# Optimization experiments

Measured on AMD Instinct MI355X. Metric: run time of the kernel, lower is better.

Reference implementation:

```python
import jax, jax.numpy as jnp
import numpy as np

HIDDEN, LATENT, SYM, BOX = 512, 256, 64, 128
LEAF = 16384
NODE = 2 * LEAF - 1  # 32767: complete binary tree, leaves first
W_SCALE = 0.05  # keep tanh unsaturated


def setup_inputs() -> dict:
    key = jax.random.key(0)
    ks = jax.random.split(key, 16)
    # kids: valid tree structure (randint per-spec would give invalid child pointers).
    # Leaves are nodes [0, LEAF); internal node LEAF+j merges nodes 2j and 2j+1
    # (1-indexed pointers 2j+1, 2j+2). Every 4th internal node is a symmetry node.
    j = np.arange(NODE - LEAF)
    kids = np.zeros((1, NODE, 3), dtype=np.int32)
    kids[0, LEAF:, 0] = 2 * j + 1
    kids[0, LEAF:, 1] = 2 * j + 2
    kids[0, LEAF:, 2] = (j % 4 == 3).astype(np.int32)
    f32 = jnp.float32
    return {
        "kids": jnp.asarray(kids),
        "shape": jax.random.normal(ks[0], (1, BOX, LEAF), dtype=f32),
        "param": jax.random.normal(ks[1], (1, NODE, SYM), dtype=f32),
        # leaf / box encoder: box -> latent
        "Wb": jax.random.normal(ks[2], (BOX, LATENT), dtype=f32) * W_SCALE,
        "bb": jnp.zeros((LATENT,), dtype=f32),
        # adjacency encoder: (latent, latent) -> hidden -> latent
        "Wl": jax.random.normal(ks[3], (LATENT, HIDDEN), dtype=f32) * W_SCALE,
        "Wr": jax.random.normal(ks[4], (LATENT, HIDDEN), dtype=f32) * W_SCALE,
        "b1": jnp.zeros((HIDDEN,), dtype=f32),
        "W2": jax.random.normal(ks[5], (HIDDEN, LATENT), dtype=f32) * W_SCALE,
        "b2": jnp.zeros((LATENT,), dtype=f32),
        # symmetry encoder: (latent, sym) -> hidden -> latent
        "Wsl": jax.random.normal(ks[6], (LATENT, HIDDEN), dtype=f32) * W_SCALE,
        "Wsr": jax.random.normal(ks[7], (SYM, HIDDEN), dtype=f32) * W_SCALE,
        "bs1": jnp.zeros((HIDDEN,), dtype=f32),
        "Ws2": jax.random.normal(ks[8], (HIDDEN, LATENT), dtype=f32) * W_SCALE,
        "bs2": jnp.zeros((LATENT,), dtype=f32),
    }


def reference(kids, shape, param, Wb, bb, Wl, Wr, b1, W2, b2, Wsl, Wsr, bs1, Ws2, bs2):
    nodeNum = kids.shape[1]
    leafNum = shape.shape[2]
    latent = Wb.shape[1]

    # Leaves (nodes 0..leafNum-1, kids[...,0]==0) have no data dependence on hOut:
    # encode them all at once. boxes: [leafNum, box]
    boxes = jnp.transpose(shape[0])
    hLeaf = jnp.tanh(boxes @ Wb + bb)  # [leafNum, latent]
    hOut = jnp.zeros((nodeNum, latent), dtype=shape.dtype).at[:leafNum].set(hLeaf)

    p = param[0]  # [nodeNum, sym]
    k = kids[0]   # [nodeNum, 3]

    def step(h, x):
        i, k0, k1, k2 = x
        a = h[k0 - 1]      # [latent] left child hidden
        b = h[k1 - 1]      # [latent] right child hidden (adjacency case)
        s = p[k0 - 1]      # [sym]    (source indexes param with kids[...,0]-1)
        # adjacency merge
        h1 = jnp.tanh(jnp.tanh(a @ Wl + b @ Wr + b1) @ W2 + b2)
        # symmetry merge
        h2 = jnp.tanh(jnp.tanh(a @ Wsl + s @ Wsr + bs1) @ Ws2 + bs2)
        hi = jnp.where(k2 == 1, h2, h1)
        return h.at[i].set(hi), None

    # internal nodes are i in [leafNum, nodeNum); original only defines inputs there
    idx = jnp.arange(leafNum, nodeNum)
    xs = (idx, k[leafNum:, 0], k[leafNum:, 1], k[leafNum:, 2])
    hOut, _ = jax.lax.scan(step, hOut, xs)
    return hOut[nodeNum - 1][None, :]  # [1, latent], the root code
```

## Files before the change

### kernel.cpp

```cpp
#include <hip/hip_runtime.h>

#define LEAF   16384
#define NNODE  (2*LEAF-1)
#define LATENT 256
#define HIDDEN 512
#define SYM    64
#define BOX    128

using half8 = __attribute__((ext_vector_type(8))) _Float16;
using f32x4 = __attribute__((ext_vector_type(4))) float;

__device__ __forceinline__ f32x4 mfma16h(half8 a, half8 b, f32x4 c){
    return __builtin_amdgcn_mfma_f32_16x16x32_f16(a, b, c, 0, 0, 0);
}

__global__ void pack_all(const float* __restrict__ Wl, const float* __restrict__ Wr,
                         const float* __restrict__ Wsl, const float* __restrict__ Wsr,
                         const float* __restrict__ W2, const float* __restrict__ Ws2,
                         const float* __restrict__ Wb,
                         _Float16* __restrict__ wcat, _Float16* __restrict__ wscat,
                         _Float16* __restrict__ w2p, _Float16* __restrict__ ws2p,
                         _Float16* __restrict__ wbp)
{
    int g = blockIdx.x*256 + threadIdx.x;
    const float *A, *B; _Float16* pk; int Ksplit, N, KS, t;
    if (g < 262144)      { t = g;          A=Wl;  B=Wr;  pk=wcat;  Ksplit=256; N=512; KS=16; }
    else if (g < 425984) { t = g-262144;   A=Wsl; B=Wsr; pk=wscat; Ksplit=256; N=512; KS=10; }
    else if (g < 557056) { t = g-425984;   A=W2;  B=W2;  pk=w2p;   Ksplit=512; N=256; KS=16; }
    else if (g < 688128) { t = g-557056;   A=Ws2; B=Ws2; pk=ws2p;  Ksplit=512; N=256; KS=16; }
    else if (g < 720896) { t = g-688128;   A=Wb;  B=Wb;  pk=wbp;   Ksplit=128; N=256; KS=4;  }
    else return;
    int j = t & 7, l = (t>>3)&63, tile = (t>>9)&3;
    int rest = t >> 11;
    int ks = rest % KS, cb = rest / KS;
    int k   = ks*32 + ((l>>4)*8) + j;
    int col = cb*64 + tile*16 + (l&15);
    float wv = (k < Ksplit) ? A[(size_t)k*N + col] : B[(size_t)(k-Ksplit)*N + col];
    pk[((size_t)(cb*KS + ks)*4 + tile)*512 + (size_t)l*8 + j] = (_Float16)wv;
}

__global__ __launch_bounds__(256) void leaf_mfma_kernel(
    const float* __restrict__ shape, const _Float16* __restrict__ wbpk,
    const float* __restrict__ bb, _Float16* __restrict__ hh)
{
    const int t = threadIdx.x, lane = t & 63, w = t >> 6;
    const int r0 = blockIdx.x * 64;
    const int m = r0 + w*16 + (lane & 15);

    half8 A[4];
    #pragma unroll
    for (int ks = 0; ks < 4; ++ks) {
        #pragma unroll
        for (int e = 0; e < 8; ++e) {
            int k = ks*32 + (lane >> 4)*8 + e;
            A[ks][e] = (_Float16)shape[(size_t)k*LEAF + m];
        }
    }

    for (int cb = 0; cb < 4; ++cb) {
        f32x4 acc[4];
        #pragma unroll
        for (int c = 0; c < 4; ++c) acc[c] = (f32x4){0.f,0.f,0.f,0.f};
        #pragma unroll
        for (int ks = 0; ks < 4; ++ks) {
            const _Float16* pb = wbpk + (size_t)((cb*4 + ks)*4)*512;
            #pragma unroll
            for (int tile = 0; tile < 4; ++tile) {
                half8 B = *(const half8*)(pb + tile*512 + lane*8);
                acc[tile] = mfma16h(A[ks], B, acc[tile]);
            }
        }
        #pragma unroll
        for (int tile = 0; tile < 4; ++tile) {
            int col = cb*64 + tile*16 + (lane & 15);
            float bv = bb[col];
            #pragma unroll
            for (int r = 0; r < 4; ++r) {
                int row = r0 + w*16 + (lane >> 4)*4 + r;
                hh[(size_t)row*256 + col] = (_Float16)tanhf(acc[tile][r] + bv);
            }
        }
    }
}

template<int NSUB>
__device__ __forceinline__ void k1_body(
    int rb, int cb, int start, int n,
    const _Float16* __restrict__ hh, const float* __restrict__ param,
    const _Float16* __restrict__ wcatpk, const _Float16* __restrict__ wscatpk,
    const float* __restrict__ b1, const float* __restrict__ bs1,
    _Float16* __restrict__ U, _Float16* __restrict__ V)
{
    __shared__ __align__(16) _Float16 ldsB1[2*2048];
    const int t = threadIdx.x, lane = t & 63, w = t >> 6;
    const bool isV = cb >= 8;
    const int cbl = isV ? cb - 8 : cb;
    const int KS  = isV ? 10 : 16;
    const _Float16* pk = (isV ? wscatpk : wcatpk) + (size_t)cbl * KS * 2048;
    const int row0  = rb * NSUB * 64;
    const int cbase = 2 * (start - LEAF);

    f32x4 acc[NSUB][4];
    #pragma unroll
    for (int s = 0; s < NSUB; ++s)
        #pragma unroll
        for (int c = 0; c < 4; ++c) acc[s][c] = (f32x4){0.f,0.f,0.f,0.f};

    *(half8*)(ldsB1 + t*8) = *(const half8*)(pk + (size_t)t*8);
    __syncthreads();

    for (int ks = 0; ks < KS; ++ks) {
        const bool hasNext = ks + 1 < KS;
        half8 stg;
        if (hasNext) stg = *(const half8*)(pk + (size_t)(ks+1)*2048 + (size_t)t*8);
        half8 A[NSUB];
        #pragma unroll
        for (int s = 0; s < NSUB; ++s) {
            int m = row0 + (s*4 + w)*16 + (lane & 15);
            if (m >= n) m = n - 1;
            if (!isV || ks < 8) {
                int node = cbase + 2*m + (ks >= 8 ? 1 : 0);
                A[s] = *(const half8*)(hh + (size_t)node*256 + (size_t)(ks & 7)*32 + ((lane >> 4)*8));
            } else {
                const float* pp = param + (size_t)(cbase + 2*m)*64 + (ks - 8)*32 + (lane >> 4)*8;
                float4 p0 = *(const float4*)pp;
                float4 p1 = *(const float4*)(pp + 4);
                A[s][0]=(_Float16)p0.x; A[s][1]=(_Float16)p0.y; A[s][2]=(_Float16)p0.z; A[s][3]=(_Float16)p0.w;
                A[s][4]=(_Float16)p1.x; A[s][5]=(_Float16)p1.y; A[s][6]=(_Float16)p1.z; A[s][7]=(_Float16)p1.w;
            }
        }
        const _Float16* lb = ldsB1 + (ks & 1)*2048;
        #pragma unroll
        for (int tile = 0; tile < 4; ++tile) {
            half8 Bh = *(const half8*)(lb + tile*512 + lane*8);
            #pragma unroll
            for (int s = 0; s < NSUB; ++s)
                acc[s][tile] = mfma16h(A[s], Bh, acc[s][tile]);
        }
        if (hasNext)
            *(half8*)(ldsB1 + ((ks+1) & 1)*2048 + t*8) = stg;
        __syncthreads();
    }

    const float* bias = isV ? bs1 : b1;
    _Float16* o = isV ? V : U;
    #pragma unroll
    for (int s = 0; s < NSUB; ++s) {
        #pragma unroll
        for (int tile = 0; tile < 4; ++tile) {
            int col = cbl*64 + tile*16 + (lane & 15);
            float bv = bias[col];
            #pragma unroll
            for (int r = 0; r < 4; ++r) {
                int m = row0 + (s*4 + w)*16 + (lane >> 4)*4 + r;
                if (m < n)
                    o[(size_t)m*512 + col] = (_Float16)tanhf(acc[s][tile][r] + bv);
            }
        }
    }
}

template<int NSUB>
__device__ __forceinline__ void k2_body(
    int rb, int cb, int start, int n,
    const _Float16* __restrict__ U, const _Float16* __restrict__ V,
    const int* __restrict__ kids,
    const _Float16* __restrict__ w2pk, const _Float16* __restrict__ ws2pk,
    const float* __restrict__ b2, const float* __restrict__ bs2,
    _Float16* __restrict__ hh)
{
    __shared__ __align__(16) _Float16 ldsB2[2*2048];
    const int t = threadIdx.x, lane = t & 63, w = t >> 6;
    const bool isSym = cb >= 4;
    const int cbl = isSym ? cb - 4 : cb;
    const _Float16* pk = (isSym ? ws2pk : w2pk) + (size_t)cbl * 16 * 2048;
    const _Float16* Asrc = isSym ? V : U;
    const int row0 = rb * NSUB * 64;

    f32x4 acc[NSUB][4];
    #pragma unroll
    for (int s = 0; s < NSUB; ++s)
        #pragma unroll
        for (int c = 0; c < 4; ++c) acc[s][c] = (f32x4){0.f,0.f,0.f,0.f};

    *(half8*)(ldsB2 + t*8) = *(const half8*)(pk + (size_t)t*8);
    __syncthreads();

    for (int ks = 0; ks < 16; ++ks) {
        const bool hasNext = ks + 1 < 16;
        half8 stg;
        if (hasNext) stg = *(const half8*)(pk + (size_t)(ks+1)*2048 + (size_t)t*8);
        half8 A[NSUB];
        #pragma unroll
        for (int s = 0; s < NSUB; ++s) {
            int m = row0 + (s*4 + w)*16 + (lane & 15);
            if (m >= n) m = n - 1;
            A[s] = *(const half8*)(Asrc + (size_t)m*512 + (size_t)ks*32 + ((lane >> 4)*8));
        }
        const _Float16* lb = ldsB2 + (ks & 1)*2048;
        #pragma unroll
        for (int tile = 0; tile < 4; ++tile) {
            half8 Bh = *(const half8*)(lb + tile*512 + lane*8);
            #pragma unroll
            for (int s = 0; s < NSUB; ++s)
                acc[s][tile] = mfma16h(A[s], Bh, acc[s][tile]);
        }
        if (hasNext)
            *(half8*)(ldsB2 + ((ks+1) & 1)*2048 + t*8) = stg;
        __syncthreads();
    }

    const float* bias = isSym ? bs2 : b2;
    const int want = isSym ? 1 : 0;
    #pragma unroll
    for (int s = 0; s < NSUB; ++s) {
        #pragma unroll
        for (int tile = 0; tile < 4; ++tile) {
            int col = cbl*64 + tile*16 + (lane & 15);
            float bv = bias[col];
            #pragma unroll
            for (int r = 0; r < 4; ++r) {
                int m = row0 + (s*4 + w)*16 + (lane >> 4)*4 + r;
                if (m < n && kids[3*(start + m) + 2] == want)
                    hh[(size_t)(start + m)*256 + col] = (_Float16)tanhf(acc[s][tile][r] + bv);
            }
        }
    }
}

template<int NSUB>
__global__ __launch_bounds__(256) void k1_kernel(
    const _Float16* __restrict__ hh, const float* __restrict__ param,
    const _Float16* __restrict__ wcatpk, const _Float16* __restrict__ wscatpk,
    const float* __restrict__ b1, const float* __restrict__ bs1,
    _Float16* __restrict__ U, _Float16* __restrict__ V, int start, int n)
{
    k1_body<NSUB>(blockIdx.x, blockIdx.y, start, n, hh, param, wcatpk, wscatpk, b1, bs1, U, V);
}

template<int NSUB>
__global__ __launch_bounds__(256) void k2_kernel(
    const _Float16* __restrict__ U, const _Float16* __restrict__ V,
    const int* __restrict__ kids,
    const _Float16* __restrict__ w2pk, const _Float16* __restrict__ ws2pk,
    const float* __restrict__ b2, const float* __restrict__ bs2,
    _Float16* __restrict__ hh, int start, int n)
{
    k2_body<NSUB>(blockIdx.x, blockIdx.y, start, n, U, V, kids, w2pk, ws2pk, b2, bs2, hh);
}

__device__ __forceinline__ void k1_tail(
    int rb, int cb, int start, int n,
    const _Float16* __restrict__ hh, const float* __restrict__ param,
    const _Float16* wlds, f32x4 bv,
    _Float16* __restrict__ U, _Float16* __restrict__ V)
{
    const int t = threadIdx.x, lane = t & 63, w = t >> 6;
    const bool isV = cb >= 8;
    const int cbl = isV ? cb - 8 : cb;
    const int KS  = isV ? 10 : 16;
    const int row0  = rb * 64;
    const int cbase = 2 * (start - LEAF);

    f32x4 acc[4];
    #pragma unroll
    for (int c = 0; c < 4; ++c) acc[c] = (f32x4){0.f,0.f,0.f,0.f};

    int m = row0 + w*16 + (lane & 15);
    if (m >= n) m = n - 1;

    for (int ks = 0; ks < KS; ++ks) {
        half8 A;
        if (!isV || ks < 8) {
            int node = cbase + 2*m + (ks >= 8 ? 1 : 0);
            A = __builtin_nontemporal_load(
                (const half8*)(hh + (size_t)node*256 + (size_t)(ks & 7)*32 + ((lane >> 4)*8)));
        } else {
            const float* pp = param + (size_t)(cbase + 2*m)*64 + (ks - 8)*32 + (lane >> 4)*8;
            f32x4 p0 = __builtin_nontemporal_load((const f32x4*)pp);
            f32x4 p1 = __builtin_nontemporal_load((const f32x4*)(pp + 4));
            A[0]=(_Float16)p0[0]; A[1]=(_Float16)p0[1]; A[2]=(_Float16)p0[2]; A[3]=(_Float16)p0[3];
            A[4]=(_Float16)p1[0]; A[5]=(_Float16)p1[1]; A[6]=(_Float16)p1[2]; A[7]=(_Float16)p1[3];
        }
        const _Float16* lb = wlds + ks*2048;
        #pragma unroll
        for (int tile = 0; tile < 4; ++tile) {
            half8 Bh = *(const half8*)(lb + tile*512 + lane*8);
            acc[tile] = mfma16h(A, Bh, acc[tile]);
        }
    }

    _Float16* o = isV ? V : U;
    #pragma unroll
    for (int tile = 0; tile < 4; ++tile) {
        int col = cbl*64 + tile*16 + (lane & 15);
        #pragma unroll
        for (int r = 0; r < 4; ++r) {
            int mm = row0 + w*16 + (lane >> 4)*4 + r;
            if (mm < n)
                __builtin_nontemporal_store(
                    (_Float16)tanhf(acc[tile][r] + bv[tile]), o + (size_t)mm*512 + col);
        }
    }
}

__device__ __forceinline__ void k2_tail(
    int rb, int cb, int start, int n,
    const _Float16* __restrict__ U, const _Float16* __restrict__ V,
    const int* __restrict__ kids,
    const _Float16* wlds, f32x4 bv,
    _Float16* __restrict__ hh)
{
    const int t = threadIdx.x, lane = t & 63, w = t >> 6;
    const bool isSym = cb >= 4;
    const int cbl = isSym ? cb - 4 : cb;
    const _Float16* Asrc = isSym ? V : U;
    const int row0 = rb * 64;

    f32x4 acc[4];
    #pragma unroll
    for (int c = 0; c < 4; ++c) acc[c] = (f32x4){0.f,0.f,0.f,0.f};

    int m = row0 + w*16 + (lane & 15);
    if (m >= n) m = n - 1;

    for (int ks = 0; ks < 16; ++ks) {
        half8 A = __builtin_nontemporal_load(
            (const half8*)(Asrc + (size_t)m*512 + (size_t)ks*32 + ((lane >> 4)*8)));
        const _Float16* lb = wlds + ks*2048;
        #pragma unroll
        for (int tile = 0; tile < 4; ++tile) {
            half8 Bh = *(const half8*)(lb + tile*512 + lane*8);
            acc[tile] = mfma16h(A, Bh, acc[tile]);
        }
    }

    const int want = isSym ? 1 : 0;
    #pragma unroll
    for (int tile = 0; tile < 4; ++tile) {
        int col = cbl*64 + tile*16 + (lane & 15);
        #pragma unroll
        for (int r = 0; r < 4; ++r) {
            int mm = row0 + w*16 + (lane >> 4)*4 + r;
            if (mm < n) {
                int k2v = __builtin_nontemporal_load(kids + 3*(start + mm) + 2);
                if (k2v == want)
                    __builtin_nontemporal_store(
                        (_Float16)tanhf(acc[tile][r] + bv[tile]), hh + (size_t)(start + mm)*256 + col);
            }
        }
    }
}

#define TAILG 48
__device__ __forceinline__ void fbar(unsigned* flags, unsigned tgt)
{
    __syncthreads();
    if (threadIdx.x == 0)
        __hip_atomic_store(flags + blockIdx.x*16, tgt, __ATOMIC_RELEASE, __HIP_MEMORY_SCOPE_AGENT);
    if (threadIdx.x < TAILG) {
        while (__hip_atomic_load(flags + threadIdx.x*16, __ATOMIC_RELAXED, __HIP_MEMORY_SCOPE_AGENT) < tgt)
            __builtin_amdgcn_s_sleep(1);
    }
    __syncthreads();
    __builtin_amdgcn_fence(__ATOMIC_ACQUIRE, "agent");
}

__global__ __launch_bounds__(256) void tail_kernel(
    _Float16* __restrict__ hh, const float* __restrict__ param,
    const _Float16* __restrict__ wcatpk, const _Float16* __restrict__ wscatpk,
    const float* __restrict__ b1, const float* __restrict__ bs1,
    _Float16* __restrict__ U, _Float16* __restrict__ V,
    const int* __restrict__ kids,
    const _Float16* __restrict__ w2pk, const _Float16* __restrict__ ws2pk,
    const float* __restrict__ b2, const float* __restrict__ bs2,
    unsigned* __restrict__ flags, float* __restrict__ out)
{
    __shared__ __align__(16) _Float16 wlds[16*2048];
    const int b = blockIdx.x;
    const int t = threadIdx.x, lane = t & 63;
    const bool isK1 = b < 32;
    int cb, rh;
    const _Float16* src;
    const float* bias;
    int nh;
    if (isK1) {
        cb = b & 15; rh = b >> 4;
        if (cb < 8) { src = wcatpk  + (size_t)cb*16*2048;     nh = 16*256; bias = b1; }
        else        { src = wscatpk + (size_t)(cb-8)*10*2048; nh = 10*256; bias = bs1; }
    } else {
        int i = b - 32; cb = i & 7; rh = i >> 3;
        if (cb < 4) { src = w2pk  + (size_t)cb*16*2048;     bias = b2; }
        else        { src = ws2pk + (size_t)(cb-4)*16*2048; bias = bs2; }
        nh = 16*256;
    }
    for (int i = t; i < nh; i += 256)
        *(half8*)(wlds + (size_t)i*8) = *(const half8*)(src + (size_t)i*8);

    f32x4 bv;
    {
        int cbl = isK1 ? (cb & 7) : (cb & 3);
        #pragma unroll
        for (int tile = 0; tile < 4; ++tile)
            bv[tile] = bias[cbl*64 + tile*16 + (lane & 15)];
    }
    __syncthreads();

    unsigned tgt = 0;
    int start = LEAF + 8192 + 4096 + 2048 + 1024 + 512;
    for (int n = 256; n >= 1; n >>= 1) {
        int rt = (n + 63) >> 6;
        if (isK1) {
            for (int r = rh; r < rt; r += 2)
                k1_tail(r, cb, start, n, hh, param, wlds, bv, U, V);
        }
        ++tgt; fbar(flags, tgt);
        if (!isK1) {
            for (int r = rh; r < rt; r += 2)
                k2_tail(r, cb, start, n, U, V, kids, wlds, bv, hh);
        }
        ++tgt; fbar(flags, tgt);
        start += n;
    }
    if (b == 0)
        out[t] = (float)hh[(size_t)(NNODE - 1)*256 + t];
}

extern "C" void kernel_launch(void* const* d_in, const int* in_sizes, int n_in,
                              void* d_out, int out_size, void* d_ws, size_t ws_size,
                              hipStream_t stream) {
    const int*   kids  = (const int*)  d_in[0];
    const float* shape = (const float*)d_in[1];
    const float* param = (const float*)d_in[2];
    const float* Wb    = (const float*)d_in[3];
    const float* bb    = (const float*)d_in[4];
    const float* Wl    = (const float*)d_in[5];
    const float* Wr    = (const float*)d_in[6];
    const float* b1    = (const float*)d_in[7];
    const float* W2    = (const float*)d_in[8];
    const float* b2    = (const float*)d_in[9];
    const float* Wsl   = (const float*)d_in[10];
    const float* Wsr   = (const float*)d_in[11];
    const float* bs1   = (const float*)d_in[12];
    const float* Ws2   = (const float*)d_in[13];
    const float* bs2   = (const float*)d_in[14];
    float* out = (float*)d_out;

    char* ws = (char*)d_ws;
    _Float16* hh      = (_Float16*)(ws + 0);
    _Float16* U       = (_Float16*)(ws + 16777216);
    _Float16* V       = (_Float16*)(ws + 25165824);
    _Float16* wcatpk  = (_Float16*)(ws + 33554432);
    _Float16* wscatpk = (_Float16*)(ws + 34078720);
    _Float16* w2pk    = (_Float16*)(ws + 34406400);
    _Float16* ws2pk   = (_Float16*)(ws + 34668544);
    _Float16* wbpk    = (_Float16*)(ws + 34930688);
    unsigned* flags   = (unsigned*)(ws + 34996224);

    hipMemsetAsync(flags, 0, TAILG*64, stream);

    pack_all<<<2816, 256, 0, stream>>>(Wl, Wr, Wsl, Wsr, W2, Ws2, Wb,
                                       wcatpk, wscatpk, w2pk, ws2pk, wbpk);

    leaf_mfma_kernel<<<LEAF/64, 256, 0, stream>>>(shape, wbpk, bb, hh);

    int start = LEAF;
    for (int n = 8192; n >= 512; n >>= 1) {
        if (n == 8192) {
            k1_kernel<2><<<dim3(n/128, 16), 256, 0, stream>>>(hh, param, wcatpk, wscatpk,
                                                              b1, bs1, U, V, start, n);
        } else {
            k1_kernel<1><<<dim3(n/64, 16), 256, 0, stream>>>(hh, param, wcatpk, wscatpk,
                                                             b1, bs1, U, V, start, n);
        }
        k2_kernel<1><<<dim3(n/64, 8), 256, 0, stream>>>(U, V, kids, w2pk, ws2pk,
                                                        b2, bs2, hh, start, n);
        start += n;
    }

    tail_kernel<<<TAILG, 256, 0, stream>>>(hh, param, wcatpk, wscatpk, b1, bs1,
                                           U, V, kids, w2pk, ws2pk, b2, bs2, flags, out);
}
```

Before: 400.1 us.

## Extend persistent tail kernel to two more levels and lighten barrier fences

Moves the 1024 and 512 node levels from separate k1/k2 launches into the persistent 48-block tail kernel, which removes four kernel launches. Inside the tail kernel, global reads now use relaxed agent-scope atomic loads issued up front into register arrays so all loads are in flight before the MFMAs. Blocks that wrote nothing in a phase publish their flag with a relaxed store, and the post-barrier acquire fence drops from agent to workgroup scope. The 48 blocks now handle more rows per level than the wider launches did, and correctness relies on the atomic loads bypassing stale cache given the weaker fence.

```diff
diff --git a/kernel.cpp b/kernel.cpp
--- a/kernel.cpp
+++ b/kernel.cpp
@@ -12,6 +12,13 @@
 
 __device__ __forceinline__ f32x4 mfma16h(half8 a, half8 b, f32x4 c){
     return __builtin_amdgcn_mfma_f32_16x16x32_f16(a, b, c, 0, 0, 0);
+}
+
+__device__ __forceinline__ half8 ldc16(const _Float16* p){
+    union { unsigned long long u[2]; half8 h; } c;
+    c.u[0] = __hip_atomic_load((const unsigned long long*)p,     __ATOMIC_RELAXED, __HIP_MEMORY_SCOPE_AGENT);
+    c.u[1] = __hip_atomic_load((const unsigned long long*)p + 1, __ATOMIC_RELAXED, __HIP_MEMORY_SCOPE_AGENT);
+    return c.h;
 }
 
 __global__ void pack_all(const float* __restrict__ Wl, const float* __restrict__ Wr,
@@ -258,35 +265,53 @@
     const int t = threadIdx.x, lane = t & 63, w = t >> 6;
     const bool isV = cb >= 8;
     const int cbl = isV ? cb - 8 : cb;
-    const int KS  = isV ? 10 : 16;
     const int row0  = rb * 64;
     const int cbase = 2 * (start - LEAF);
 
-    f32x4 acc[4];
-    #pragma unroll
-    for (int c = 0; c < 4; ++c) acc[c] = (f32x4){0.f,0.f,0.f,0.f};
-
     int m = row0 + w*16 + (lane & 15);
     if (m >= n) m = n - 1;
 
-    for (int ks = 0; ks < KS; ++ks) {
-        half8 A;
-        if (!isV || ks < 8) {
+    f32x4 acc[4];
+    #pragma unroll
+    for (int c = 0; c < 4; ++c) acc[c] = (f32x4){0.f,0.f,0.f,0.f};
+
+    if (!isV) {
+        half8 A[16];
+        #pragma unroll
+        for (int ks = 0; ks < 16; ++ks) {
             int node = cbase + 2*m + (ks >= 8 ? 1 : 0);
-            A = __builtin_nontemporal_load(
-                (const half8*)(hh + (size_t)node*256 + (size_t)(ks & 7)*32 + ((lane >> 4)*8)));
-        } else {
+            A[ks] = ldc16(hh + (size_t)node*256 + (size_t)(ks & 7)*32 + ((lane >> 4)*8));
+        }
+        #pragma unroll
+        for (int ks = 0; ks < 16; ++ks) {
+            const _Float16* lb = wlds + ks*2048;
+            #pragma unroll
+            for (int tile = 0; tile < 4; ++tile) {
+                half8 Bh = *(const half8*)(lb + tile*512 + lane*8);
+                acc[tile] = mfma16h(A[ks], Bh, acc[tile]);
+            }
+        }
+    } else {
+        half8 A[10];
+        #pragma unroll
+        for (int ks = 0; ks < 8; ++ks)
+            A[ks] = ldc16(hh + (size_t)(cbase + 2*m)*256 + (size_t)ks*32 + ((lane >> 4)*8));
+        #pragma unroll
+        for (int ks = 8; ks < 10; ++ks) {
             const float* pp = param + (size_t)(cbase + 2*m)*64 + (ks - 8)*32 + (lane >> 4)*8;
-            f32x4 p0 = __builtin_nontemporal_load((const f32x4*)pp);
-            f32x4 p1 = __builtin_nontemporal_load((const f32x4*)(pp + 4));
-            A[0]=(_Float16)p0[0]; A[1]=(_Float16)p0[1]; A[2]=(_Float16)p0[2]; A[3]=(_Float16)p0[3];
-            A[4]=(_Float16)p1[0]; A[5]=(_Float16)p1[1]; A[6]=(_Float16)p1[2]; A[7]=(_Float16)p1[3];
-        }
-        const _Float16* lb = wlds + ks*2048;
-        #pragma unroll
-        for (int tile = 0; tile < 4; ++tile) {
-            half8 Bh = *(const half8*)(lb + tile*512 + lane*8);
-            acc[tile] = mfma16h(A, Bh, acc[tile]);
+            float4 p0 = *(const float4*)pp;
+            float4 p1 = *(const float4*)(pp + 4);
+            A[ks][0]=(_Float16)p0.x; A[ks][1]=(_Float16)p0.y; A[ks][2]=(_Float16)p0.z; A[ks][3]=(_Float16)p0.w;
+            A[ks][4]=(_Float16)p1.x; A[ks][5]=(_Float16)p1.y; A[ks][6]=(_Float16)p1.z; A[ks][7]=(_Float16)p1.w;
+        }
+        #pragma unroll
+        for (int ks = 0; ks < 10; ++ks) {
+            const _Float16* lb = wlds + ks*2048;
+            #pragma unroll
+            for (int tile = 0; tile < 4; ++tile) {
+                half8 Bh = *(const half8*)(lb + tile*512 + lane*8);
+                acc[tile] = mfma16h(A[ks], Bh, acc[tile]);
+            }
         }
     }
 
@@ -298,8 +323,7 @@
         for (int r = 0; r < 4; ++r) {
             int mm = row0 + w*16 + (lane >> 4)*4 + r;
             if (mm < n)
-                __builtin_nontemporal_store(
-                    (_Float16)tanhf(acc[tile][r] + bv[tile]), o + (size_t)mm*512 + col);
+                o[(size_t)mm*512 + col] = (_Float16)tanhf(acc[tile][r] + bv[tile]);
         }
     }
 }
@@ -317,21 +341,24 @@
     const _Float16* Asrc = isSym ? V : U;
     const int row0 = rb * 64;
 
-    f32x4 acc[4];
-    #pragma unroll
-    for (int c = 0; c < 4; ++c) acc[c] = (f32x4){0.f,0.f,0.f,0.f};
-
     int m = row0 + w*16 + (lane & 15);
     if (m >= n) m = n - 1;
 
+    half8 A[16];
+    #pragma unroll
+    for (int ks = 0; ks < 16; ++ks)
+        A[ks] = ldc16(Asrc + (size_t)m*512 + (size_t)ks*32 + ((lane >> 4)*8));
+
+    f32x4 acc[4];
+    #pragma unroll
+    for (int c = 0; c < 4; ++c) acc[c] = (f32x4){0.f,0.f,0.f,0.f};
+    #pragma unroll
     for (int ks = 0; ks < 16; ++ks) {
-        half8 A = __builtin_nontemporal_load(
-            (const half8*)(Asrc + (size_t)m*512 + (size_t)ks*32 + ((lane >> 4)*8)));
         const _Float16* lb = wlds + ks*2048;
         #pragma unroll
         for (int tile = 0; tile < 4; ++tile) {
             half8 Bh = *(const half8*)(lb + tile*512 + lane*8);
-            acc[tile] = mfma16h(A, Bh, acc[tile]);
+            acc[tile] = mfma16h(A[ks], Bh, acc[tile]);
         }
     }
 
@@ -342,28 +369,28 @@
         #pragma unroll
         for (int r = 0; r < 4; ++r) {
             int mm = row0 + w*16 + (lane >> 4)*4 + r;
-            if (mm < n) {
-                int k2v = __builtin_nontemporal_load(kids + 3*(start + mm) + 2);
-                if (k2v == want)
-                    __builtin_nontemporal_store(
-                        (_Float16)tanhf(acc[tile][r] + bv[tile]), hh + (size_t)(start + mm)*256 + col);
-            }
+            if (mm < n && kids[3*(start + mm) + 2] == want)
+                hh[(size_t)(start + mm)*256 + col] = (_Float16)tanhf(acc[tile][r] + bv[tile]);
         }
     }
 }
 
 #define TAILG 48
-__device__ __forceinline__ void fbar(unsigned* flags, unsigned tgt)
+__device__ __forceinline__ void fbar(unsigned* flags, unsigned tgt, bool wrote)
 {
     __syncthreads();
-    if (threadIdx.x == 0)
-        __hip_atomic_store(flags + blockIdx.x*16, tgt, __ATOMIC_RELEASE, __HIP_MEMORY_SCOPE_AGENT);
+    if (threadIdx.x == 0) {
+        if (wrote)
+            __hip_atomic_store(flags + blockIdx.x*16, tgt, __ATOMIC_RELEASE, __HIP_MEMORY_SCOPE_AGENT);
+        else
+            __hip_atomic_store(flags + blockIdx.x*16, tgt, __ATOMIC_RELAXED, __HIP_MEMORY_SCOPE_AGENT);
+    }
     if (threadIdx.x < TAILG) {
         while (__hip_atomic_load(flags + threadIdx.x*16, __ATOMIC_RELAXED, __HIP_MEMORY_SCOPE_AGENT) < tgt)
             __builtin_amdgcn_s_sleep(1);
     }
     __syncthreads();
-    __builtin_amdgcn_fence(__ATOMIC_ACQUIRE, "agent");
+    __builtin_amdgcn_fence(__ATOMIC_ACQUIRE, "workgroup");
 }
 
 __global__ __launch_bounds__(256) void tail_kernel(
@@ -407,23 +434,27 @@
     __syncthreads();
 
     unsigned tgt = 0;
-    int start = LEAF + 8192 + 4096 + 2048 + 1024 + 512;
-    for (int n = 256; n >= 1; n >>= 1) {
+    int start = LEAF + 8192 + 4096 + 2048;
+    for (int n = 1024; n >= 1; n >>= 1) {
         int rt = (n + 63) >> 6;
         if (isK1) {
             for (int r = rh; r < rt; r += 2)
                 k1_tail(r, cb, start, n, hh, param, wlds, bv, U, V);
         }
-        ++tgt; fbar(flags, tgt);
+        ++tgt; fbar(flags, tgt, isK1);
         if (!isK1) {
             for (int r = rh; r < rt; r += 2)
                 k2_tail(r, cb, start, n, U, V, kids, wlds, bv, hh);
         }
-        ++tgt; fbar(flags, tgt);
+        ++tgt; fbar(flags, tgt, !isK1);
         start += n;
     }
-    if (b == 0)
-        out[t] = (float)hh[(size_t)(NNODE - 1)*256 + t];
+    if (b == 0 && t < 32) {
+        half8 v = ldc16(hh + (size_t)(NNODE - 1)*256 + t*8);
+        #pragma unroll
+        for (int e = 0; e < 8; ++e)
+            out[t*8 + e] = (float)v[e];
+    }
 }
 
 extern "C" void kernel_launch(void* const* d_in, const int* in_sizes, int n_in,
@@ -465,7 +496,7 @@
     leaf_mfma_kernel<<<LEAF/64, 256, 0, stream>>>(shape, wbpk, bb, hh);
 
     int start = LEAF;
-    for (int n = 8192; n >= 512; n >>= 1) {
+    for (int n = 8192; n >= 2048; n >>= 1) {
         if (n == 8192) {
             k1_kernel<2><<<dim3(n/128, 16), 256, 0, stream>>>(hh, param, wcatpk, wscatpk,
                                                               b1, bs1, U, V, start, n);
```

Result: slower. 416.3 us (+4.1%).
